# Kernel tuning notes

Hardware: AMD Instinct MI355X
Metric: run time of the kernel (lower is better)

Reference implementation:

```python
import jax, jax.numpy as jnp
import numpy as np

K = 10          # nearest neighbors per ligand atom
BN_EPS = 1e-5   # torch BatchNorm1d default eps


def _pool_one(pos, feats, lig):
    """pos:(N,3) feats:(N,D) lig:(M,3) -> (D,) mean over unique kNN indices."""
    # squared distances give the same top-k indices as cdist (monotone)
    d2 = (jnp.sum(pos * pos, -1, keepdims=True)
          + jnp.sum(lig * lig, -1)[None, :]
          - 2.0 * (pos @ lig.T))                      # (N, M)
    d2 = jax.lax.stop_gradient(d2)                    # mirrors torch.no_grad
    idx = jax.lax.top_k(-d2.T, K)[1]                  # (M, K) nearest vertex ids per atom
    # unique(idx) then mean == masked mean over the set of selected vertices
    mask = jnp.zeros(pos.shape[0], feats.dtype).at[idx.reshape(-1)].set(1.0)  # (N,)
    return (mask @ feats) / jnp.sum(mask)             # (D,)


def setup_inputs() -> dict:
    key = jax.random.key(0)
    ks = jax.random.split(key, 6)
    B, N, M, D, C = 32, 8192, 64, 512, 7
    return {
        "pos": jax.random.normal(ks[0], (B, N, 3), jnp.float32) * 10.0,
        "feats": jax.random.normal(ks[1], (B, N, D), jnp.float32),
        "lig_coords": jax.random.normal(ks[2], (B, M, 3), jnp.float32) * 10.0,
        "W1": jax.random.normal(ks[3], (D, D), jnp.float32) / np.sqrt(D),
        "b1": jnp.zeros((D,), jnp.float32),
        "gamma": jnp.ones((D,), jnp.float32),
        "beta": jnp.zeros((D,), jnp.float32),
        "W2": jax.random.normal(ks[4], (C, D), jnp.float32) / np.sqrt(D),
        "b2": jnp.zeros((C,), jnp.float32),
    }


def reference(pos, feats, lig_coords, W1, b1, gamma, beta, W2, b2):
    # per-sample kNN pooling around ligand atoms -> (B, D)
    x = jax.vmap(_pool_one)(pos, feats, lig_coords)
    # classifier: Linear -> Dropout(identity in eval) -> BatchNorm1d(batch stats) -> SiLU -> Linear
    h = x @ W1.T + b1
    mu = jnp.mean(h, axis=0)
    var = jnp.var(h, axis=0)
    h = gamma * (h - mu) * jax.lax.rsqrt(var + BN_EPS) + beta
    h = jax.nn.silu(h)
    return h @ W2.T + b2
```

## Files before the change

kernel.cpp:

```cpp
#include <hip/hip_runtime.h>
#include <cfloat>
#include <climits>
#include <math.h>

#define NVERT 8192
#define NATOM 64
#define KNN   10
#define DIM   512
#define BATCH 32
#define NCLS  7
#define BN_EPS 1e-5f

__global__ __launch_bounds__(256) void knn_kernel(
    const float* __restrict__ pos,
    const float* __restrict__ lig,
    int* __restrict__ topk)
{
    const int bm  = blockIdx.x;
    const int b   = bm >> 6;
    const int m   = bm & 63;
    const int tid = threadIdx.x;

    const float* p = pos + (size_t)b * NVERT * 3;
    const float* l = lig + ((size_t)b * NATOM + m) * 3;
    const float lx = l[0], ly = l[1], lz = l[2];
    const float l2 = lx * lx + ly * ly + lz * lz;

    float bd[KNN];
    int   bi[KNN];
#pragma unroll
    for (int i = 0; i < KNN; ++i) { bd[i] = FLT_MAX; bi[i] = INT_MAX; }

    for (int n = tid; n < NVERT; n += 256) {
        const float px = p[n * 3 + 0];
        const float py = p[n * 3 + 1];
        const float pz = p[n * 3 + 2];
        const float d2 = (px * px + py * py + pz * pz) + l2
                         - 2.0f * (px * lx + py * ly + pz * lz);
        if (d2 < bd[KNN - 1]) {
            bd[KNN - 1] = d2;
            bi[KNN - 1] = n;
#pragma unroll
            for (int j = KNN - 1; j > 0; --j) {
                const bool sw = (bd[j] < bd[j - 1]) ||
                                (bd[j] == bd[j - 1] && bi[j] < bi[j - 1]);
                if (sw) {
                    float td = bd[j]; bd[j] = bd[j - 1]; bd[j - 1] = td;
                    int   ti = bi[j]; bi[j] = bi[j - 1]; bi[j - 1] = ti;
                }
            }
        }
    }

    __shared__ float sD[256 * KNN];
    __shared__ int   sI[256 * KNN];
#pragma unroll
    for (int i = 0; i < KNN; ++i) {
        sD[tid * KNN + i] = bd[i];
        sI[tid * KNN + i] = bi[i];
    }

    __shared__ float rD[256];
    __shared__ int   rI[256];

    int head = 0;
    int* out = topk + (size_t)bm * KNN;

    for (int r = 0; r < KNN; ++r) {
        const float cd = (head < KNN) ? sD[tid * KNN + head] : FLT_MAX;
        const int   ci = (head < KNN) ? sI[tid * KNN + head] : INT_MAX;
        rD[tid] = cd;
        rI[tid] = ci;
        __syncthreads();
        for (int s = 128; s > 0; s >>= 1) {
            if (tid < s) {
                const float od = rD[tid + s];
                const int   oi = rI[tid + s];
                if (od < rD[tid] || (od == rD[tid] && oi < rI[tid])) {
                    rD[tid] = od;
                    rI[tid] = oi;
                }
            }
            __syncthreads();
        }
        const int win = rI[0];
        if (tid == 0) out[r] = win;
        if (ci == win) head++;
        __syncthreads();
    }
}

__global__ __launch_bounds__(512) void pool_kernel(
    const float* __restrict__ feats,
    const int* __restrict__ topk,
    float* __restrict__ x)
{
    const int b   = blockIdx.x;
    const int tid = threadIdx.x;

    __shared__ unsigned char mask[NVERT];
    __shared__ int list[NATOM * KNN];
    __shared__ int cnt;

    for (int n = tid; n < NVERT; n += 512) mask[n] = 0;
    if (tid == 0) cnt = 0;
    __syncthreads();

    const int* tk = topk + (size_t)b * NATOM * KNN;
    for (int j = tid; j < NATOM * KNN; j += 512) mask[tk[j]] = 1;
    __syncthreads();

    for (int n = tid; n < NVERT; n += 512) {
        if (mask[n]) {
            const int pp = atomicAdd(&cnt, 1);
            list[pp] = n;
        }
    }
    __syncthreads();

    const int count = cnt;
    const float* fb = feats + (size_t)b * NVERT * DIM;
    float acc = 0.0f;
    for (int j = 0; j < count; ++j) {
        acc += fb[(size_t)list[j] * DIM + tid];
    }
    x[(size_t)b * DIM + tid] = acc / (float)count;
}

__global__ __launch_bounds__(512) void fc1_kernel(
    const float* __restrict__ x,
    const float* __restrict__ W1,
    const float* __restrict__ b1,
    float* __restrict__ h)
{
    const int b = blockIdx.x;
    const int d = threadIdx.x;

    __shared__ float xs[DIM];
    xs[d] = x[(size_t)b * DIM + d];
    __syncthreads();

    const float4* wr = (const float4*)(W1 + (size_t)d * DIM);
    float acc = b1[d];
#pragma unroll 4
    for (int k4 = 0; k4 < DIM / 4; ++k4) {
        const float4 w = wr[k4];
        acc += xs[4 * k4 + 0] * w.x + xs[4 * k4 + 1] * w.y +
               xs[4 * k4 + 2] * w.z + xs[4 * k4 + 3] * w.w;
    }
    h[(size_t)b * DIM + d] = acc;
}

__global__ __launch_bounds__(512) void bnstats_kernel(
    const float* __restrict__ h,
    float* __restrict__ mu,
    float* __restrict__ var)
{
    const int d = threadIdx.x;
    float s = 0.0f;
    for (int b = 0; b < BATCH; ++b) s += h[(size_t)b * DIM + d];
    const float m = s * (1.0f / BATCH);
    float q = 0.0f;
    for (int b = 0; b < BATCH; ++b) {
        const float t = h[(size_t)b * DIM + d] - m;
        q += t * t;
    }
    mu[d]  = m;
    var[d] = q * (1.0f / BATCH);
}

__global__ __launch_bounds__(512) void head_kernel(
    const float* __restrict__ h,
    const float* __restrict__ mu,
    const float* __restrict__ var,
    const float* __restrict__ gamma,
    const float* __restrict__ beta,
    const float* __restrict__ W2,
    const float* __restrict__ b2,
    float* __restrict__ out)
{
    const int b   = blockIdx.x;
    const int tid = threadIdx.x;

    __shared__ float s[DIM];
    const float v  = h[(size_t)b * DIM + tid];
    const float hn = gamma[tid] * (v - mu[tid]) * rsqrtf(var[tid] + BN_EPS)
                     + beta[tid];
    s[tid] = hn / (1.0f + expf(-hn));
    __syncthreads();

    const int w    = tid >> 6;
    const int lane = tid & 63;
    if (w < NCLS) {
        float acc = 0.0f;
        for (int d = lane; d < DIM; d += 64)
            acc += s[d] * W2[(size_t)w * DIM + d];
        for (int off = 32; off > 0; off >>= 1)
            acc += __shfl_down(acc, off);
        if (lane == 0) out[(size_t)b * NCLS + w] = acc + b2[w];
    }
}

extern "C" void kernel_launch(void* const* d_in, const int* in_sizes, int n_in,
                              void* d_out, int out_size, void* d_ws, size_t ws_size,
                              hipStream_t stream)
{
    const float* pos   = (const float*)d_in[0];
    const float* feats = (const float*)d_in[1];
    const float* lig   = (const float*)d_in[2];
    const float* W1    = (const float*)d_in[3];
    const float* b1    = (const float*)d_in[4];
    const float* gamma = (const float*)d_in[5];
    const float* beta  = (const float*)d_in[6];
    const float* W2    = (const float*)d_in[7];
    const float* b2    = (const float*)d_in[8];
    float* out = (float*)d_out;

    char* ws = (char*)d_ws;
    int*   topk = (int*)ws;
    float* x    = (float*)(ws + 81920);
    float* h    = (float*)(ws + 81920 + 65536);
    float* mu   = (float*)(ws + 81920 + 65536 + 65536);
    float* var  = (float*)(ws + 81920 + 65536 + 65536 + 2048);

    knn_kernel<<<BATCH * NATOM, 256, 0, stream>>>(pos, lig, topk);
    pool_kernel<<<BATCH, 512, 0, stream>>>(feats, topk, x);
    fc1_kernel<<<BATCH, 512, 0, stream>>>(x, W1, b1, h);
    bnstats_kernel<<<1, 512, 0, stream>>>(h, mu, var);
    head_kernel<<<BATCH, 512, 0, stream>>>(h, mu, var, gamma, beta, W2, b2, out);
}
```

Measured before the change: 799.0 us.

## Split pooling gather across chunked blocks and use wave-shuffle top-k merge

The kNN merge now runs a wave-level shuffle reduction per wave, then a final 40-candidate merge in a single wave. This replaces the 256-thread shared-memory tree reduction and its many barriers. Pooling is split into a list-building kernel and a gather kernel that spreads each batch's selected rows over 16 blocks with four independent accumulators. The fc1 kernel sums the partial results and divides by the count. This exposes far more parallelism for the feature gather, which previously ran on only 32 blocks, at the cost of an extra launch and partial-sum traffic.

```diff
diff --git a/kernel.cpp b/kernel.cpp
--- a/kernel.cpp
+++ b/kernel.cpp
@@ -9,6 +9,7 @@
 #define DIM   512
 #define BATCH 32
 #define NCLS  7
+#define CH    16
 #define BN_EPS 1e-5f
 
 __global__ __launch_bounds__(256) void knn_kernel(
@@ -16,10 +17,12 @@
     const float* __restrict__ lig,
     int* __restrict__ topk)
 {
-    const int bm  = blockIdx.x;
-    const int b   = bm >> 6;
-    const int m   = bm & 63;
-    const int tid = threadIdx.x;
+    const int bm   = blockIdx.x;
+    const int b    = bm >> 6;
+    const int m    = bm & 63;
+    const int tid  = threadIdx.x;
+    const int lane = tid & 63;
+    const int wave = tid >> 6;
 
     const float* p = pos + (size_t)b * NVERT * 3;
     const float* l = lig + ((size_t)b * NATOM + m) * 3;
@@ -52,83 +55,109 @@
         }
     }
 
-    __shared__ float sD[256 * KNN];
-    __shared__ int   sI[256 * KNN];
-#pragma unroll
-    for (int i = 0; i < KNN; ++i) {
-        sD[tid * KNN + i] = bd[i];
-        sI[tid * KNN + i] = bi[i];
-    }
-
-    __shared__ float rD[256];
-    __shared__ int   rI[256];
-
-    int head = 0;
-    int* out = topk + (size_t)bm * KNN;
+    __shared__ float sD[4 * KNN];
+    __shared__ int   sI[4 * KNN];
 
     for (int r = 0; r < KNN; ++r) {
-        const float cd = (head < KNN) ? sD[tid * KNN + head] : FLT_MAX;
-        const int   ci = (head < KNN) ? sI[tid * KNN + head] : INT_MAX;
-        rD[tid] = cd;
-        rI[tid] = ci;
-        __syncthreads();
-        for (int s = 128; s > 0; s >>= 1) {
-            if (tid < s) {
-                const float od = rD[tid + s];
-                const int   oi = rI[tid + s];
-                if (od < rD[tid] || (od == rD[tid] && oi < rI[tid])) {
-                    rD[tid] = od;
-                    rI[tid] = oi;
-                }
+        float cd = bd[0];
+        int   ci = bi[0];
+#pragma unroll
+        for (int off = 1; off < 64; off <<= 1) {
+            const float od = __shfl_xor(cd, off);
+            const int   oi = __shfl_xor(ci, off);
+            if (od < cd || (od == cd && oi < ci)) { cd = od; ci = oi; }
+        }
+        if (lane == 0) { sD[wave * KNN + r] = cd; sI[wave * KNN + r] = ci; }
+        if (bi[0] == ci) {
+#pragma unroll
+            for (int j = 0; j < KNN - 1; ++j) { bd[j] = bd[j + 1]; bi[j] = bi[j + 1]; }
+            bd[KNN - 1] = FLT_MAX;
+            bi[KNN - 1] = INT_MAX;
+        }
+    }
+    __syncthreads();
+
+    if (wave == 0) {
+        float cd = (lane < 4 * KNN) ? sD[lane] : FLT_MAX;
+        int   ci = (lane < 4 * KNN) ? sI[lane] : INT_MAX;
+        int* out = topk + (size_t)bm * KNN;
+        for (int r = 0; r < KNN; ++r) {
+            float wd = cd;
+            int   wi = ci;
+#pragma unroll
+            for (int off = 1; off < 64; off <<= 1) {
+                const float od = __shfl_xor(wd, off);
+                const int   oi = __shfl_xor(wi, off);
+                if (od < wd || (od == wd && oi < wi)) { wd = od; wi = oi; }
             }
-            __syncthreads();
-        }
-        const int win = rI[0];
-        if (tid == 0) out[r] = win;
-        if (ci == win) head++;
-        __syncthreads();
-    }
-}
-
-__global__ __launch_bounds__(512) void pool_kernel(
-    const float* __restrict__ feats,
+            if (lane == 0) out[r] = wi;
+            if (ci == wi) { cd = FLT_MAX; ci = INT_MAX; }
+        }
+    }
+}
+
+__global__ __launch_bounds__(512) void pool_list_kernel(
     const int* __restrict__ topk,
-    float* __restrict__ x)
+    int* __restrict__ list,
+    int* __restrict__ cnt)
 {
     const int b   = blockIdx.x;
     const int tid = threadIdx.x;
 
     __shared__ unsigned char mask[NVERT];
-    __shared__ int list[NATOM * KNN];
-    __shared__ int cnt;
+    __shared__ int c;
 
     for (int n = tid; n < NVERT; n += 512) mask[n] = 0;
-    if (tid == 0) cnt = 0;
+    if (tid == 0) c = 0;
     __syncthreads();
 
     const int* tk = topk + (size_t)b * NATOM * KNN;
     for (int j = tid; j < NATOM * KNN; j += 512) mask[tk[j]] = 1;
     __syncthreads();
 
+    int* lb = list + (size_t)b * (NATOM * KNN);
     for (int n = tid; n < NVERT; n += 512) {
-        if (mask[n]) {
-            const int pp = atomicAdd(&cnt, 1);
-            list[pp] = n;
-        }
-    }
-    __syncthreads();
-
-    const int count = cnt;
-    const float* fb = feats + (size_t)b * NVERT * DIM;
-    float acc = 0.0f;
-    for (int j = 0; j < count; ++j) {
-        acc += fb[(size_t)list[j] * DIM + tid];
-    }
-    x[(size_t)b * DIM + tid] = acc / (float)count;
+        if (mask[n]) lb[atomicAdd(&c, 1)] = n;
+    }
+    __syncthreads();
+    if (tid == 0) cnt[b] = c;
+}
+
+__global__ __launch_bounds__(512) void pool_gather_kernel(
+    const float* __restrict__ feats,
+    const int* __restrict__ list,
+    const int* __restrict__ cnt,
+    float* __restrict__ partial)
+{
+    const int bc  = blockIdx.x;
+    const int b   = bc / CH;
+    const int c   = bc % CH;
+    const int tid = threadIdx.x;
+
+    const int count  = cnt[b];
+    const int* lb    = list + (size_t)b * (NATOM * KNN);
+    const float* fb  = feats + (size_t)b * NVERT * DIM;
+
+    float a0 = 0.f, a1 = 0.f, a2 = 0.f, a3 = 0.f;
+    int j = c;
+    for (; j + 3 * CH < count; j += 4 * CH) {
+        const int i0 = lb[j];
+        const int i1 = lb[j + CH];
+        const int i2 = lb[j + 2 * CH];
+        const int i3 = lb[j + 3 * CH];
+        a0 += fb[(size_t)i0 * DIM + tid];
+        a1 += fb[(size_t)i1 * DIM + tid];
+        a2 += fb[(size_t)i2 * DIM + tid];
+        a3 += fb[(size_t)i3 * DIM + tid];
+    }
+    for (; j < count; j += CH) a0 += fb[(size_t)lb[j] * DIM + tid];
+
+    partial[((size_t)b * CH + c) * DIM + tid] = (a0 + a1) + (a2 + a3);
 }
 
 __global__ __launch_bounds__(512) void fc1_kernel(
-    const float* __restrict__ x,
+    const float* __restrict__ partial,
+    const int* __restrict__ cnt,
     const float* __restrict__ W1,
     const float* __restrict__ b1,
     float* __restrict__ h)
@@ -137,7 +166,11 @@
     const int d = threadIdx.x;
 
     __shared__ float xs[DIM];
-    xs[d] = x[(size_t)b * DIM + d];
+    float s = 0.f;
+#pragma unroll
+    for (int c = 0; c < CH; ++c)
+        s += partial[((size_t)b * CH + c) * DIM + d];
+    xs[d] = s / (float)cnt[b];
     __syncthreads();
 
     const float4* wr = (const float4*)(W1 + (size_t)d * DIM);
@@ -217,15 +250,18 @@
     float* out = (float*)d_out;
 
     char* ws = (char*)d_ws;
-    int*   topk = (int*)ws;
-    float* x    = (float*)(ws + 81920);
-    float* h    = (float*)(ws + 81920 + 65536);
-    float* mu   = (float*)(ws + 81920 + 65536 + 65536);
-    float* var  = (float*)(ws + 81920 + 65536 + 65536 + 2048);
+    int*   topk    = (int*)(ws + 0);
+    int*   list    = (int*)(ws + 81920);
+    int*   cnt     = (int*)(ws + 163840);
+    float* partial = (float*)(ws + 196608);
+    float* h       = (float*)(ws + 196608 + 1048576);
+    float* mu      = (float*)(ws + 196608 + 1048576 + 65536);
+    float* var     = (float*)(ws + 196608 + 1048576 + 65536 + 2048);
 
     knn_kernel<<<BATCH * NATOM, 256, 0, stream>>>(pos, lig, topk);
-    pool_kernel<<<BATCH, 512, 0, stream>>>(feats, topk, x);
-    fc1_kernel<<<BATCH, 512, 0, stream>>>(x, W1, b1, h);
+    pool_list_kernel<<<BATCH, 512, 0, stream>>>(topk, list, cnt);
+    pool_gather_kernel<<<BATCH * CH, 512, 0, stream>>>(feats, list, cnt, partial);
+    fc1_kernel<<<BATCH, 512, 0, stream>>>(partial, cnt, W1, b1, h);
     bnstats_kernel<<<1, 512, 0, stream>>>(h, mu, var);
     head_kernel<<<BATCH, 512, 0, stream>>>(h, mu, var, gamma, beta, W2, b2, out);
 }
```

Measured after the change: 762.6 us. 4.6% less time.
